# Kernel tuning notes

Hardware: AMD Instinct MI355X
Metric: run time of the kernel (lower is better)

The kernel has to match this reference:

```python
import jax, jax.numpy as jnp
import numpy as np

N = 50000      # nodes
E = 250000     # edges
D = 256        # in_channels
MSG = 256      # msg_dim
TD = 64        # time encoder out_channels
ED = MSG + TD  # edge_dim = 320
H = 4          # heads
C = 64         # out_channels // heads


def setup_inputs() -> dict:
    key = jax.random.key(0)
    ks = jax.random.split(key, 16)
    s_d = 1.0 / np.sqrt(D)
    s_e = 1.0 / np.sqrt(ED)
    return {
        "x": jax.random.normal(ks[0], (N, D), jnp.float32),
        "last_update": jax.random.uniform(ks[1], (N,), jnp.float32) * 1000.0,
        "t": jax.random.uniform(ks[2], (E,), jnp.float32) * 1000.0,
        "msg": jax.random.normal(ks[3], (E, MSG), jnp.float32),
        "edge_index": jax.random.randint(ks[4], (2, E), 0, N, jnp.int32),
        # TimeEncoder: Linear(1, TD) followed by cos
        "time_w": jax.random.normal(ks[5], (TD,), jnp.float32),
        "time_b": jax.random.normal(ks[6], (TD,), jnp.float32) * 0.1,
        # TransformerConv linears (weights stored [out, in] like torch)
        "Wq": jax.random.normal(ks[7], (H * C, D), jnp.float32) * s_d,
        "bq": jnp.zeros((H * C,), jnp.float32),
        "Wk": jax.random.normal(ks[8], (H * C, D), jnp.float32) * s_d,
        "bk": jnp.zeros((H * C,), jnp.float32),
        "Wv": jax.random.normal(ks[9], (H * C, D), jnp.float32) * s_d,
        "bv": jnp.zeros((H * C,), jnp.float32),
        "We": jax.random.normal(ks[10], (H * C, ED), jnp.float32) * s_e,  # lin_edge, no bias
        "Wskip": jax.random.normal(ks[11], (H * C, D), jnp.float32) * s_d,
        "bskip": jnp.zeros((H * C,), jnp.float32),
    }


def reference(x, last_update, t, msg, edge_index, time_w, time_b,
              Wq, bq, Wk, bk, Wv, bv, We, Wskip, bskip):
    src = edge_index[0]  # j: message source
    dst = edge_index[1]  # i: message target

    # time encoding: cos(Linear(1, TD)(rel_t))
    rel_t = last_update[src] - t                              # [E]
    rel_t_enc = jnp.cos(rel_t[:, None] * time_w[None, :] + time_b)  # [E, TD]
    edge_attr = jnp.concatenate([rel_t_enc, msg], axis=-1)    # [E, ED]

    # TransformerConv (heads=4, concat=True, root_weight=True, beta=False, eval mode)
    q = (x @ Wq.T + bq).reshape(N, H, C)
    k = (x @ Wk.T + bk).reshape(N, H, C)
    v = (x @ Wv.T + bv).reshape(N, H, C)
    e = (edge_attr @ We.T).reshape(E, H, C)

    k_j = k[src] + e                                           # [E, H, C]
    alpha = jnp.einsum('ehc,ehc->eh', q[dst], k_j) / np.sqrt(C)  # [E, H]

    # segment softmax over incoming edges of each target node
    m = jax.ops.segment_max(alpha, dst, num_segments=N)        # [N, H]
    m = jnp.where(jnp.isfinite(m), m, 0.0)
    ex = jnp.exp(alpha - m[dst])                               # [E, H]
    denom = jax.ops.segment_sum(ex, dst, num_segments=N)       # [N, H]
    alpha = ex / (denom[dst] + 1e-16)                          # [E, H]

    out_e = (v[src] + e) * alpha[:, :, None]                   # [E, H, C]
    out = jax.ops.segment_sum(out_e, dst, num_segments=N)      # [N, H, C]
    out = out.reshape(N, H * C) + (x @ Wskip.T + bskip)        # skip connection
    return out
```

## Files before the change

### kernel.cpp

```cpp
#include <hip/hip_runtime.h>
#include <math.h>

#define NN 50000
#define EE 250000

typedef float f32x4 __attribute__((ext_vector_type(4)));
typedef __bf16 bf16x8 __attribute__((ext_vector_type(8)));

static __device__ __forceinline__ ushort f2b(float f) {
    __bf16 h = (__bf16)f;
    return *(ushort*)&h;
}
static __device__ __forceinline__ float b2f(ushort u) {
    return __uint_as_float(((unsigned)u) << 16);
}

typedef __attribute__((address_space(1))) const unsigned int gu32;
typedef __attribute__((address_space(3))) unsigned int lu32;
static __device__ __forceinline__ void gl2lds16(const void* g, void* l) {
    __builtin_amdgcn_global_load_lds((gu32*)g, (lu32*)l, 16, 0, 0);
}

__global__ void k_prep_w(const float* __restrict__ Wq, const float* __restrict__ bq,
                         const float* __restrict__ Wk, const float* __restrict__ bk,
                         const float* __restrict__ Wv, const float* __restrict__ bv,
                         const float* __restrict__ Wskip, const float* __restrict__ bskip,
                         const float* __restrict__ We,
                         ushort* __restrict__ Wnb_sw, ushort* __restrict__ Web_sw,
                         float* __restrict__ bcat, unsigned* __restrict__ deg) {
    int i = blockIdx.x * 256 + threadIdx.x;
    int st = gridDim.x * 256;
    for (int ch = i; ch < 16 * 2048; ch += st) {
        int tile = ch >> 11, pc = ch & 2047;
        int r = pc >> 5, sc = pc & 31;
        int c = (sc & 24) | ((sc ^ r) & 7);
        int n = tile * 64 + r, sel = n >> 8, o = n & 255;
        const float* W = (sel == 0) ? Wq : (sel == 1) ? Wk : (sel == 2) ? Wv : Wskip;
        const float* src = W + o * 256 + c * 8;
        union { ushort u[8]; uint4 v; } s;
        #pragma unroll
        for (int j = 0; j < 8; ++j) s.u[j] = f2b(src[j]);
        *(uint4*)&Wnb_sw[(size_t)ch * 8] = s.v;
    }
    for (int ch = i; ch < 5 * 2048; ch += st) {
        int ks = ch >> 11, pc = ch & 2047;
        int r = pc >> 3, q = pc & 7;
        int c = q ^ (r & 7);
        const float* src = We + r * 320 + ks * 64 + c * 8;
        union { ushort u[8]; uint4 v; } s;
        #pragma unroll
        for (int j = 0; j < 8; ++j) s.u[j] = f2b(src[j]);
        *(uint4*)&Web_sw[(size_t)ch * 8] = s.v;
    }
    for (int idx = i; idx < 1024; idx += st) {
        int sel = idx >> 8, o = idx & 255;
        const float* b = (sel == 0) ? bq : (sel == 1) ? bk : (sel == 2) ? bv : bskip;
        bcat[idx] = b[o];
    }
    for (int idx = i; idx < NN; idx += st) deg[idx] = 0u;
}

__global__ void k_hist(const int* __restrict__ ei, unsigned* __restrict__ deg) {
    int i = blockIdx.x * 256 + threadIdx.x;
    if (i < EE) atomicAdd(&deg[ei[EE + i]], 1u);
}

__global__ __launch_bounds__(1024) void k_scan(const unsigned* __restrict__ deg,
                                               unsigned* __restrict__ offs,
                                               unsigned* __restrict__ cursor) {
    __shared__ unsigned part[1024];
    int t = threadIdx.x;
    const int CH = (NN + 1023) / 1024;
    int b0 = t * CH;
    unsigned s = 0;
    for (int i = 0; i < CH; ++i) { int idx = b0 + i; if (idx < NN) s += deg[idx]; }
    part[t] = s;
    __syncthreads();
    for (int d = 1; d < 1024; d <<= 1) {
        unsigned v = (t >= d) ? part[t - d] : 0u;
        __syncthreads();
        part[t] += v;
        __syncthreads();
    }
    unsigned run = (t == 0) ? 0u : part[t - 1];
    for (int i = 0; i < CH; ++i) {
        int idx = b0 + i;
        if (idx < NN) { offs[idx] = run; cursor[idx] = run; run += deg[idx]; }
    }
    if (t == 1023) offs[NN] = EE;
}

__global__ void k_scatter(const int* __restrict__ ei, unsigned* __restrict__ cursor,
                          int* __restrict__ rank) {
    int i = blockIdx.x * 256 + threadIdx.x;
    if (i < EE) {
        unsigned p = atomicAdd(&cursor[ei[EE + i]], 1u);
        rank[i] = (int)p;
    }
}

__global__ __launch_bounds__(256) void k_node_mfma(
        const float* __restrict__ x, const ushort* __restrict__ Wnb_sw,
        const float* __restrict__ bcat,
        ushort* __restrict__ qb, ushort* __restrict__ kb, ushort* __restrict__ vb,
        float* __restrict__ out) {
    __shared__ ushort As[64 * 256];
    __shared__ ushort Bs[64 * 256];
    int tid = threadIdx.x;
    int lane = tid & 63, wid = tid >> 6;
    int wrow = wid >> 1, wcol = wid & 1;
    int li = lane & 15, g = lane >> 4;
    int bm = blockIdx.x;
    #pragma unroll
    for (int i = 0; i < 8; ++i) {
        int ch = tid + i * 256;
        int r = ch >> 5, c = ch & 31;
        int row = bm * 64 + r;
        union { ushort u[8]; uint4 v; } s;
        if (row < NN) {
            const float* xr = x + (size_t)row * 256 + c * 8;
            float4 a = *(const float4*)xr;
            float4 b = *(const float4*)(xr + 4);
            s.u[0] = f2b(a.x); s.u[1] = f2b(a.y); s.u[2] = f2b(a.z); s.u[3] = f2b(a.w);
            s.u[4] = f2b(b.x); s.u[5] = f2b(b.y); s.u[6] = f2b(b.z); s.u[7] = f2b(b.w);
        } else {
            s.v = make_uint4(0, 0, 0, 0);
        }
        int sc = (c & 24) | ((c ^ r) & 7);
        *(uint4*)&As[r * 256 + sc * 8] = s.v;
    }
    for (int bng2 = 0; bng2 < 16; ++bng2) {
        __syncthreads();
        #pragma unroll
        for (int i = 0; i < 8; ++i) {
            int pcb = (i * 4 + wid) * 64;
            gl2lds16(Wnb_sw + ((size_t)bng2 * 2048 + pcb + lane) * 8, &Bs[pcb * 8]);
        }
        __syncthreads();
        f32x4 acc[2][2] = {};
        #pragma unroll
        for (int ks = 0; ks < 8; ++ks) {
            bf16x8 a[2], b[2];
            int c = ks * 4 + g;
            #pragma unroll
            for (int m = 0; m < 2; ++m) {
                int r = wrow * 32 + m * 16 + li;
                int sc = (c & 24) | ((c ^ r) & 7);
                a[m] = *(const bf16x8*)&As[r * 256 + sc * 8];
            }
            #pragma unroll
            for (int n = 0; n < 2; ++n) {
                int r = wcol * 32 + n * 16 + li;
                int sc = (c & 24) | ((c ^ r) & 7);
                b[n] = *(const bf16x8*)&Bs[r * 256 + sc * 8];
            }
            #pragma unroll
            for (int m = 0; m < 2; ++m)
                #pragma unroll
                for (int n = 0; n < 2; ++n)
                    acc[m][n] = __builtin_amdgcn_mfma_f32_16x16x32_bf16(a[m], b[n], acc[m][n], 0, 0, 0);
        }
        int sel = bng2 >> 2;
        int cbase = (bng2 & 3) * 64;
        ushort* dstb = (sel == 0) ? qb : (sel == 1) ? kb : vb;
        #pragma unroll
        for (int m = 0; m < 2; ++m) {
            #pragma unroll
            for (int r = 0; r < 4; ++r) {
                int row = bm * 64 + wrow * 32 + m * 16 + g * 4 + r;
                if (row >= NN) continue;
                #pragma unroll
                for (int n = 0; n < 2; ++n) {
                    int coll = wcol * 32 + n * 16 + li;
                    float val = acc[m][n][r] + bcat[bng2 * 64 + coll];
                    int cin = cbase + coll;
                    if (sel < 3) dstb[(size_t)row * 256 + cin] = f2b(val);
                    else         out[(size_t)row * 256 + cin] = val;
                }
            }
        }
    }
}

__global__ __launch_bounds__(256) void k_edge_mfma(
        const float* __restrict__ msg, const float* __restrict__ t_arr,
        const float* __restrict__ lu, const float* __restrict__ tw,
        const float* __restrict__ tb, const ushort* __restrict__ Web_sw,
        const ushort* __restrict__ qb, const ushort* __restrict__ kb,
        const ushort* __restrict__ vb, const int* __restrict__ ei,
        const int* __restrict__ rank,
        ushort* __restrict__ ebuf, float* __restrict__ alpha) {
    __shared__ ushort SS[64 * 328];
    __shared__ int s_src[64], s_dst[64], s_rank[64];
    __shared__ float s_relt[64];
    int tid = threadIdx.x;
    int lane = tid & 63, wid = tid >> 6;
    int wr = wid >> 1, wc = wid & 1;
    int li = lane & 15, g = lane >> 4;
    int e0 = blockIdx.x * 64;
    if (tid < 64) {
        int e = e0 + tid;
        if (e >= EE) e = EE - 1;
        int s = ei[e];
        s_src[tid] = s;
        s_dst[tid] = ei[EE + e];
        s_rank[tid] = rank[e];
        s_relt[tid] = lu[s] - t_arr[e];
    }
    f32x4 acc[2][8] = {};
    for (int ks = 0; ks < 5; ++ks) {
        int k0 = ks * 64;
        __syncthreads();
        #pragma unroll
        for (int i = 0; i < 8; ++i) {
            int pcb = (i * 4 + wid) * 64;
            gl2lds16(Web_sw + ((size_t)ks * 2048 + pcb + lane) * 8, &SS[4096 + pcb * 8]);
        }
        #pragma unroll
        for (int i = 0; i < 2; ++i) {
            int ch = tid + i * 256;
            int r = ch >> 3, c = ch & 7;
            union { ushort u[8]; uint4 v; } s;
            if (k0 == 0) {
                float rt = s_relt[r];
                #pragma unroll
                for (int j = 0; j < 8; ++j)
                    s.u[j] = f2b(cosf(rt * tw[c * 8 + j] + tb[c * 8 + j]));
            } else {
                int erow = e0 + r; if (erow >= EE) erow = EE - 1;
                const float* mrow = msg + (size_t)erow * 256 + (k0 - 64) + c * 8;
                float4 a = *(const float4*)mrow;
                float4 b = *(const float4*)(mrow + 4);
                s.u[0] = f2b(a.x); s.u[1] = f2b(a.y); s.u[2] = f2b(a.z); s.u[3] = f2b(a.w);
                s.u[4] = f2b(b.x); s.u[5] = f2b(b.y); s.u[6] = f2b(b.z); s.u[7] = f2b(b.w);
            }
            *(uint4*)&SS[r * 64 + ((c ^ (r & 7)) * 8)] = s.v;
        }
        __syncthreads();
        #pragma unroll
        for (int kk = 0; kk < 2; ++kk) {
            bf16x8 a[2], b[8];
            #pragma unroll
            for (int m = 0; m < 2; ++m) {
                int r = wr * 32 + m * 16 + li;
                a[m] = *(const bf16x8*)&SS[r * 64 + (((kk * 4 + g) ^ (r & 7)) * 8)];
            }
            #pragma unroll
            for (int n = 0; n < 8; ++n) {
                int r = wc * 128 + n * 16 + li;
                b[n] = *(const bf16x8*)&SS[4096 + r * 64 + (((kk * 4 + g) ^ (r & 7)) * 8)];
            }
            #pragma unroll
            for (int m = 0; m < 2; ++m)
                #pragma unroll
                for (int n = 0; n < 8; ++n)
                    acc[m][n] = __builtin_amdgcn_mfma_f32_16x16x32_bf16(a[m], b[n], acc[m][n], 0, 0, 0);
        }
    }
    __syncthreads();
    #pragma unroll
    for (int i = 0; i < 8; ++i) {
        int idx = tid + i * 256;
        int r = idx >> 5, c = idx & 31;
        uint4 vv = *(const uint4*)(vb + (size_t)s_src[r] * 256 + c * 8);
        *(uint4*)&SS[r * 328 + c * 8] = vv;
    }
    __syncthreads();
    #pragma unroll
    for (int m = 0; m < 2; ++m) {
        #pragma unroll
        for (int r = 0; r < 4; ++r) {
            int el = wr * 32 + m * 16 + g * 4 + r;
            int edge = e0 + el;
            if (edge >= EE) continue;
            size_t rb = (size_t)s_rank[el] * 256;
            #pragma unroll
            for (int n = 0; n < 8; ++n) {
                int col = wc * 128 + n * 16 + li;
                ebuf[rb + col] = f2b(acc[m][n][r] + b2f(SS[el * 328 + col]));
            }
        }
    }
    __syncthreads();
    #pragma unroll
    for (int i = 0; i < 8; ++i) {
        int idx = tid + i * 256;
        int r = idx >> 5, c = idx & 31;
        uint4 kv = *(const uint4*)(kb + (size_t)s_src[r] * 256 + c * 8);
        *(uint4*)&SS[r * 328 + c * 8] = kv;
    }
    __syncthreads();
    #pragma unroll
    for (int m = 0; m < 2; ++m)
        #pragma unroll
        for (int r = 0; r < 4; ++r) {
            int el = wr * 32 + m * 16 + g * 4 + r;
            #pragma unroll
            for (int n = 0; n < 8; ++n)
                acc[m][n][r] += b2f(SS[el * 328 + wc * 128 + n * 16 + li]);
        }
    __syncthreads();
    #pragma unroll
    for (int i = 0; i < 8; ++i) {
        int idx = tid + i * 256;
        int r = idx >> 5, c = idx & 31;
        uint4 qv = *(const uint4*)(qb + (size_t)s_dst[r] * 256 + c * 8);
        *(uint4*)&SS[r * 328 + c * 8] = qv;
    }
    __syncthreads();
    #pragma unroll
    for (int m = 0; m < 2; ++m) {
        #pragma unroll
        for (int r = 0; r < 4; ++r) {
            int el = wr * 32 + m * 16 + g * 4 + r;
            int edge = e0 + el;
            float p0 = 0.f, p1 = 0.f;
            #pragma unroll
            for (int n = 0; n < 8; ++n) {
                float qv = b2f(SS[el * 328 + wc * 128 + n * 16 + li]);
                float tt = qv * acc[m][n][r];
                if (n < 4) p0 += tt; else p1 += tt;
            }
            #pragma unroll
            for (int msk = 1; msk < 16; msk <<= 1) {
                p0 += __shfl_xor(p0, msk);
                p1 += __shfl_xor(p1, msk);
            }
            if (li < 2 && edge < EE) {
                float av = ((li == 0) ? p0 : p1) * 0.125f;
                int h = wc * 2 + li;
                alpha[(size_t)s_rank[el] * 4 + h] = av;
            }
        }
    }
}

__global__ __launch_bounds__(256) void k_gather(
        const ushort* __restrict__ ebuf, const float* __restrict__ alpha,
        const unsigned* __restrict__ offs, float* __restrict__ out) {
    int wid = threadIdx.x >> 6, lane = threadIdx.x & 63;
    int n = blockIdx.x * 4 + wid;
    if (n >= NN) return;
    unsigned p0 = offs[n], p1 = offs[n + 1];
    if (p0 == p1) return;
    int h = lane >> 4;
    int c0 = lane * 4;
    float m = -INFINITY;
    for (unsigned p = p0; p < p1; ++p)
        m = fmaxf(m, alpha[(size_t)p * 4 + h]);
    f32x4 acc = {0.f, 0.f, 0.f, 0.f};
    float denom = 0.f;
    for (unsigned p = p0; p < p1; ++p) {
        float ex = __expf(alpha[(size_t)p * 4 + h] - m);
        ushort4 ev = *(const ushort4*)(ebuf + (size_t)p * 256 + c0);
        acc[0] += b2f(ev.x) * ex;
        acc[1] += b2f(ev.y) * ex;
        acc[2] += b2f(ev.z) * ex;
        acc[3] += b2f(ev.w) * ex;
        denom += ex;
    }
    float inv = 1.f / (denom + 1e-16f);
    float4 o = *(float4*)(out + (size_t)n * 256 + c0);
    o.x += acc[0] * inv;
    o.y += acc[1] * inv;
    o.z += acc[2] * inv;
    o.w += acc[3] * inv;
    *(float4*)(out + (size_t)n * 256 + c0) = o;
}

extern "C" void kernel_launch(void* const* d_in, const int* in_sizes, int n_in,
                              void* d_out, int out_size, void* d_ws, size_t ws_size,
                              hipStream_t stream) {
    const float* x        = (const float*)d_in[0];
    const float* last_upd = (const float*)d_in[1];
    const float* t_arr    = (const float*)d_in[2];
    const float* msg      = (const float*)d_in[3];
    const int*   ei       = (const int*)d_in[4];
    const float* time_w   = (const float*)d_in[5];
    const float* time_b   = (const float*)d_in[6];
    const float* Wq = (const float*)d_in[7];  const float* bq = (const float*)d_in[8];
    const float* Wk = (const float*)d_in[9];  const float* bk = (const float*)d_in[10];
    const float* Wv = (const float*)d_in[11]; const float* bv = (const float*)d_in[12];
    const float* We = (const float*)d_in[13];
    const float* Wsk = (const float*)d_in[14]; const float* bsk = (const float*)d_in[15];
    float* out = (float*)d_out;
    char* base = (char*)d_ws;

    size_t off = 0;
    auto carve = [&](size_t bytes) {
        void* p = base + off;
        off += (bytes + 255) & ~(size_t)255;
        return p;
    };
    ushort* Wnb_sw = (ushort*)carve((size_t)16 * 2048 * 8 * 2);
    ushort* Web_sw = (ushort*)carve((size_t)5 * 2048 * 8 * 2);
    float*  bcat  = (float*) carve(1024 * 4);
    ushort* qb    = (ushort*)carve((size_t)NN * 256 * 2);
    ushort* kb    = (ushort*)carve((size_t)NN * 256 * 2);
    ushort* vb    = (ushort*)carve((size_t)NN * 256 * 2);
    ushort* ebuf  = (ushort*)carve((size_t)EE * 256 * 2);
    float*  alpha = (float*) carve((size_t)EE * 4 * 4);
    unsigned* deg    = (unsigned*)carve((size_t)NN * 4);
    unsigned* cursor = (unsigned*)carve((size_t)NN * 4);
    unsigned* offs   = (unsigned*)carve((size_t)(NN + 1) * 4);
    int*      rank   = (int*)     carve((size_t)EE * 4);

    k_prep_w<<<dim3(512), dim3(256), 0, stream>>>(Wq, bq, Wk, bk, Wv, bv, Wsk, bsk, We,
                                                  Wnb_sw, Web_sw, bcat, deg);
    k_hist<<<dim3((EE + 255) / 256), dim3(256), 0, stream>>>(ei, deg);
    k_scan<<<dim3(1), dim3(1024), 0, stream>>>(deg, offs, cursor);
    k_scatter<<<dim3((EE + 255) / 256), dim3(256), 0, stream>>>(ei, cursor, rank);
    k_node_mfma<<<dim3(782, 1), dim3(256), 0, stream>>>(x, Wnb_sw, bcat, qb, kb, vb, out);
    k_edge_mfma<<<dim3((EE + 63) / 64), dim3(256), 0, stream>>>(
        msg, t_arr, last_upd, time_w, time_b, Web_sw, qb, kb, vb, ei, rank, ebuf, alpha);
    k_gather<<<dim3((NN + 3) / 4), dim3(256), 0, stream>>>(ebuf, alpha, offs, out);
}
```

Before: 534.4 us.

## Double-buffer edge GEMM LDS tiles and drop shared index arrays

The edge-feature GEMM now keeps two LDS buffers for the A (time-encoding/msg) and B (We) tiles and prefetches the next k-slice while the current one is being multiplied. This replaces the two barriers per k-step with one and hides the global load latency behind the MFMA work. The per-block shared arrays for src/dst/rank/rel_t are removed, and those indices are re-read from global memory wherever they are used. LDS use grows to 80 KB per block, which may lower occupancy, and the extra index reloads add some global traffic.

Result: slower. 633.3 us (+18.5%).

```diff
diff --git a/kernel.cpp b/kernel.cpp
--- a/kernel.cpp
+++ b/kernel.cpp
@@ -190,79 +190,82 @@
         const ushort* __restrict__ vb, const int* __restrict__ ei,
         const int* __restrict__ rank,
         ushort* __restrict__ ebuf, float* __restrict__ alpha) {
-    __shared__ ushort SS[64 * 328];
-    __shared__ int s_src[64], s_dst[64], s_rank[64];
-    __shared__ float s_relt[64];
+    __shared__ ushort SS[40960];
     int tid = threadIdx.x;
     int lane = tid & 63, wid = tid >> 6;
     int wr = wid >> 1, wc = wid & 1;
     int li = lane & 15, g = lane >> 4;
     int e0 = blockIdx.x * 64;
-    if (tid < 64) {
-        int e = e0 + tid;
-        if (e >= EE) e = EE - 1;
-        int s = ei[e];
-        s_src[tid] = s;
-        s_dst[tid] = ei[EE + e];
-        s_rank[tid] = rank[e];
-        s_relt[tid] = lu[s] - t_arr[e];
-    }
     f32x4 acc[2][8] = {};
+    #pragma unroll
+    for (int i = 0; i < 8; ++i) {
+        int pcb = (i * 4 + wid) * 64;
+        gl2lds16(Web_sw + ((size_t)pcb + lane) * 8, &SS[8192 + pcb * 8]);
+    }
+    #pragma unroll
+    for (int i = 0; i < 2; ++i) {
+        int ch = tid + i * 256;
+        int r = ch >> 3, c = ch & 7;
+        int e = e0 + r; if (e >= EE) e = EE - 1;
+        float rt = lu[ei[e]] - t_arr[e];
+        union { ushort u[8]; uint4 v; } s;
+        #pragma unroll
+        for (int j = 0; j < 8; ++j)
+            s.u[j] = f2b(cosf(rt * tw[c * 8 + j] + tb[c * 8 + j]));
+        *(uint4*)&SS[r * 64 + ((c ^ (r & 7)) * 8)] = s.v;
+    }
+    __syncthreads();
     for (int ks = 0; ks < 5; ++ks) {
-        int k0 = ks * 64;
-        __syncthreads();
-        #pragma unroll
-        for (int i = 0; i < 8; ++i) {
-            int pcb = (i * 4 + wid) * 64;
-            gl2lds16(Web_sw + ((size_t)ks * 2048 + pcb + lane) * 8, &SS[4096 + pcb * 8]);
-        }
-        #pragma unroll
-        for (int i = 0; i < 2; ++i) {
-            int ch = tid + i * 256;
-            int r = ch >> 3, c = ch & 7;
-            union { ushort u[8]; uint4 v; } s;
-            if (k0 == 0) {
-                float rt = s_relt[r];
-                #pragma unroll
-                for (int j = 0; j < 8; ++j)
-                    s.u[j] = f2b(cosf(rt * tw[c * 8 + j] + tb[c * 8 + j]));
-            } else {
+        int bb = ks & 1;
+        if (ks < 4) {
+            int bn = bb ^ 1;
+            #pragma unroll
+            for (int i = 0; i < 8; ++i) {
+                int pcb = (i * 4 + wid) * 64;
+                gl2lds16(Web_sw + ((size_t)(ks + 1) * 2048 + pcb + lane) * 8,
+                         &SS[8192 + bn * 16384 + pcb * 8]);
+            }
+            #pragma unroll
+            for (int i = 0; i < 2; ++i) {
+                int ch = tid + i * 256;
+                int r = ch >> 3, c = ch & 7;
                 int erow = e0 + r; if (erow >= EE) erow = EE - 1;
-                const float* mrow = msg + (size_t)erow * 256 + (k0 - 64) + c * 8;
-                float4 a = *(const float4*)mrow;
-                float4 b = *(const float4*)(mrow + 4);
-                s.u[0] = f2b(a.x); s.u[1] = f2b(a.y); s.u[2] = f2b(a.z); s.u[3] = f2b(a.w);
-                s.u[4] = f2b(b.x); s.u[5] = f2b(b.y); s.u[6] = f2b(b.z); s.u[7] = f2b(b.w);
-            }
-            *(uint4*)&SS[r * 64 + ((c ^ (r & 7)) * 8)] = s.v;
-        }
-        __syncthreads();
+                const float* mrow = msg + (size_t)erow * 256 + ks * 64 + c * 8;
+                float4 a4 = *(const float4*)mrow;
+                float4 b4 = *(const float4*)(mrow + 4);
+                union { ushort u[8]; uint4 v; } s;
+                s.u[0] = f2b(a4.x); s.u[1] = f2b(a4.y); s.u[2] = f2b(a4.z); s.u[3] = f2b(a4.w);
+                s.u[4] = f2b(b4.x); s.u[5] = f2b(b4.y); s.u[6] = f2b(b4.z); s.u[7] = f2b(b4.w);
+                *(uint4*)&SS[bn * 4096 + r * 64 + ((c ^ (r & 7)) * 8)] = s.v;
+            }
+        }
         #pragma unroll
         for (int kk = 0; kk < 2; ++kk) {
-            bf16x8 a[2], b[8];
+            bf16x8 a[2], b8[8];
             #pragma unroll
             for (int m = 0; m < 2; ++m) {
                 int r = wr * 32 + m * 16 + li;
-                a[m] = *(const bf16x8*)&SS[r * 64 + (((kk * 4 + g) ^ (r & 7)) * 8)];
+                a[m] = *(const bf16x8*)&SS[bb * 4096 + r * 64 + (((kk * 4 + g) ^ (r & 7)) * 8)];
             }
             #pragma unroll
             for (int n = 0; n < 8; ++n) {
                 int r = wc * 128 + n * 16 + li;
-                b[n] = *(const bf16x8*)&SS[4096 + r * 64 + (((kk * 4 + g) ^ (r & 7)) * 8)];
+                b8[n] = *(const bf16x8*)&SS[8192 + bb * 16384 + r * 64 + (((kk * 4 + g) ^ (r & 7)) * 8)];
             }
             #pragma unroll
             for (int m = 0; m < 2; ++m)
                 #pragma unroll
                 for (int n = 0; n < 8; ++n)
-                    acc[m][n] = __builtin_amdgcn_mfma_f32_16x16x32_bf16(a[m], b[n], acc[m][n], 0, 0, 0);
-        }
-    }
-    __syncthreads();
+                    acc[m][n] = __builtin_amdgcn_mfma_f32_16x16x32_bf16(a[m], b8[n], acc[m][n], 0, 0, 0);
+        }
+        __syncthreads();
+    }
     #pragma unroll
     for (int i = 0; i < 8; ++i) {
         int idx = tid + i * 256;
         int r = idx >> 5, c = idx & 31;
-        uint4 vv = *(const uint4*)(vb + (size_t)s_src[r] * 256 + c * 8);
+        int e = e0 + r; if (e >= EE) e = EE - 1;
+        uint4 vv = *(const uint4*)(vb + (size_t)ei[e] * 256 + c * 8);
         *(uint4*)&SS[r * 328 + c * 8] = vv;
     }
     __syncthreads();
@@ -273,7 +276,7 @@
             int el = wr * 32 + m * 16 + g * 4 + r;
             int edge = e0 + el;
             if (edge >= EE) continue;
-            size_t rb = (size_t)s_rank[el] * 256;
+            size_t rb = (size_t)rank[edge] * 256;
             #pragma unroll
             for (int n = 0; n < 8; ++n) {
                 int col = wc * 128 + n * 16 + li;
@@ -286,7 +289,8 @@
     for (int i = 0; i < 8; ++i) {
         int idx = tid + i * 256;
         int r = idx >> 5, c = idx & 31;
-        uint4 kv = *(const uint4*)(kb + (size_t)s_src[r] * 256 + c * 8);
+        int e = e0 + r; if (e >= EE) e = EE - 1;
+        uint4 kv = *(const uint4*)(kb + (size_t)ei[e] * 256 + c * 8);
         *(uint4*)&SS[r * 328 + c * 8] = kv;
     }
     __syncthreads();
@@ -304,7 +308,8 @@
     for (int i = 0; i < 8; ++i) {
         int idx = tid + i * 256;
         int r = idx >> 5, c = idx & 31;
-        uint4 qv = *(const uint4*)(qb + (size_t)s_dst[r] * 256 + c * 8);
+        int e = e0 + r; if (e >= EE) e = EE - 1;
+        uint4 qv = *(const uint4*)(qb + (size_t)ei[EE + e] * 256 + c * 8);
         *(uint4*)&SS[r * 328 + c * 8] = qv;
     }
     __syncthreads();
@@ -329,7 +334,7 @@
             if (li < 2 && edge < EE) {
                 float av = ((li == 0) ? p0 : p1) * 0.125f;
                 int h = wc * 2 + li;
-                alpha[(size_t)s_rank[el] * 4 + h] = av;
+                alpha[(size_t)rank[edge] * 4 + h] = av;
             }
         }
     }
```
